# Kernel tuning notes

Hardware: AMD Instinct MI355X
Metric: run time of the kernel (lower is better)

Reference implementation:

```python
import jax, jax.numpy as jnp
import numpy as np

NUM_CLASS = 10000
FEATURE_DIM = 512
PARAM = 0.5


def _xavier_uniform(key, shape):
    fan_out, fan_in = shape
    bound = float(np.sqrt(6.0 / (fan_in + fan_out)))
    return jax.random.uniform(key, shape, jnp.float32, -bound, bound)


def setup_inputs() -> dict:
    key = jax.random.key(0)
    k1, k2, k3, k4, k5 = jax.random.split(key, 5)
    B = 4096
    soft_x = jax.random.normal(k1, (B, FEATURE_DIM), jnp.float32)
    hard_x = jax.random.normal(k2, (B, FEATURE_DIM), jnp.float32)
    targets = jax.random.randint(k3, (B,), 0, NUM_CLASS, jnp.int64)
    centers = _xavier_uniform(k4, (NUM_CLASS, FEATURE_DIM))
    weight = _xavier_uniform(k5, (NUM_CLASS, FEATURE_DIM))
    return {"soft_x": soft_x, "hard_x": hard_x, "targets": targets,
            "centers": centers, "weight": weight}


def _cross_entropy(logits, targets):
    # mean over batch of -log_softmax(logits)[target]
    logp = jax.nn.log_softmax(logits, axis=-1)
    return -jnp.mean(jnp.take_along_axis(logp, targets[:, None], axis=-1))


def reference(soft_x, hard_x, targets, centers, weight):
    # [B, C] logits via GEMM (F.linear -> x @ W^T)
    soft_pred = soft_x @ weight.T
    hard_pred = hard_x @ weight.T
    loss_cls1 = _cross_entropy(soft_pred, targets)
    loss_cls2 = _cross_entropy(hard_pred, targets)
    # Quantization loss: per-class loop == per-sample gather of centers
    c = centers[targets]                                # [B, D]
    quant = 0.5 * (jnp.sum((soft_x - c) ** 2) + jnp.sum((hard_x - c) ** 2))
    loss = loss_cls1 + loss_cls2 + PARAM * quant / soft_x.shape[0]
    return loss
```

## Files before the change

### kernel.cpp

```cpp
#include <hip/hip_runtime.h>
#include <stdint.h>

#define NUM_CLASS 10000
#define FEATDIM   512
#define BATCH     4096
#define MROWS     8192
#define BM        128
#define BN        128
#define NTILES    79
#define NSPLIT    12
#define ROWTILES  64
#define WPAD_ROWS 10112
#define ROWB4     256
#define KBLKS     16

#define PB_CVTX   512
#define PB_CVTW   632
#define PB_ROWS   1024
#define PB_ZERO   8
#define PB_TOTAL  (PB_CVTX + PB_CVTW + PB_ROWS + PB_ZERO)

typedef float f32x4 __attribute__((ext_vector_type(4)));
typedef int   i32x8 __attribute__((ext_vector_type(8)));

__device__ __forceinline__ void gll16(const void* g, void* l) {
  __builtin_amdgcn_global_load_lds(
      (const __attribute__((address_space(1))) void*)g,
      (__attribute__((address_space(3))) void*)l,
      16, 0, 0);
}

__device__ __forceinline__ unsigned q1(float v, float rs) {
  float a = fabsf(v) * rs;
  unsigned s = (__float_as_uint(v) >> 31) << 3;
  unsigned c = a < 0.25f ? 0u : a < 0.75f ? 1u : a < 1.25f ? 2u : a < 1.75f ? 3u
             : a < 2.5f  ? 4u : a < 3.5f  ? 5u : a < 5.0f  ? 6u : 7u;
  return s | c;
}

__device__ __forceinline__ void quant32(const float4* __restrict__ src,
                                        uint4* __restrict__ dst,
                                        unsigned char* __restrict__ sdst) {
  float4 v[8];
#pragma unroll
  for (int i = 0; i < 8; ++i) v[i] = src[i];
  float m = 0.f;
#pragma unroll
  for (int i = 0; i < 8; ++i) {
    m = fmaxf(m, fmaxf(fmaxf(fabsf(v[i].x), fabsf(v[i].y)),
                       fmaxf(fabsf(v[i].z), fabsf(v[i].w))));
  }
  unsigned sb; float rs;
  if (m == 0.f) { sb = 0u; rs = 0.f; }
  else {
    int e = (int)ceilf(log2f(m * 0.16666667f) - 1e-6f);
    e = e < -126 ? -126 : (e > 127 ? 127 : e);
    sb = (unsigned)(e + 127);
    rs = __uint_as_float((unsigned)(127 - e) << 23);
  }
  unsigned wd[4] = {0u, 0u, 0u, 0u};
#pragma unroll
  for (int i = 0; i < 8; ++i) {
    unsigned hw = q1(v[i].x, rs) | (q1(v[i].y, rs) << 4) |
                  (q1(v[i].z, rs) << 8) | (q1(v[i].w, rs) << 12);
    wd[i >> 1] |= hw << ((i & 1) * 16);
  }
  uint4 o = {wd[0], wd[1], wd[2], wd[3]};
  *dst = o;
  *sdst = (unsigned char)sb;
}

__device__ __forceinline__ int spos(int row, int blk) {
  return row * 16 + (blk & 3) * 4 + (blk >> 2);
}

__global__ void prep_kernel(const float* __restrict__ sx, const float* __restrict__ hx,
                            const int* __restrict__ tgt,
                            const float* __restrict__ centers,
                            const float* __restrict__ weight,
                            uint4* __restrict__ X4, uint4* __restrict__ W4,
                            unsigned char* __restrict__ SX, unsigned char* __restrict__ SW,
                            float* __restrict__ tlogit, float* __restrict__ qrow,
                            float4* __restrict__ sumexp4) {
  const int b   = blockIdx.x;
  const int tid = threadIdx.x;

  if (b < PB_CVTX) {
    int idx = b * 256 + tid;
    int row = idx >> 4, blk = idx & 15;
    const float* base = (row < BATCH) ? sx : hx;
    int r = (row < BATCH) ? row : row - BATCH;
    const float4* src = (const float4*)(base + (size_t)r * FEATDIM) + blk * 8;
    quant32(src, &X4[idx], &SX[spos(row, blk)]);
    return;
  }
  if (b < PB_CVTX + PB_CVTW) {
    int idx = (b - PB_CVTX) * 256 + tid;
    int row = idx >> 4, blk = idx & 15;
    if (row < NUM_CLASS) {
      const float4* src = (const float4*)(weight + (size_t)row * FEATDIM) + blk * 8;
      quant32(src, &W4[idx], &SW[spos(row, blk)]);
    } else {
      uint4 z = {0u, 0u, 0u, 0u};
      W4[idx] = z;
      SW[spos(row, blk)] = 0;
    }
    return;
  }
  if (b < PB_CVTX + PB_CVTW + PB_ROWS) {
    int row  = (b - PB_CVTX - PB_CVTW) * 4 + (tid >> 6);
    int lane = tid & 63;
    int t = tgt[row];
    const float4* s4 = (const float4*)(sx + (size_t)row * FEATDIM);
    const float4* h4 = (const float4*)(hx + (size_t)row * FEATDIM);
    const float4* c4 = (const float4*)(centers + (size_t)t * FEATDIM);
    const float4* w4 = (const float4*)(weight + (size_t)t * FEATDIM);
    float qs = 0.f, ds = 0.f, dh = 0.f;
#pragma unroll
    for (int j = 0; j < 2; ++j) {
      int i = lane + j * 64;
      float4 s = s4[i], h = h4[i], c = c4[i], w = w4[i];
      float d0 = s.x - c.x, d1 = s.y - c.y, d2 = s.z - c.z, d3 = s.w - c.w;
      float e0 = h.x - c.x, e1 = h.y - c.y, e2 = h.z - c.z, e3 = h.w - c.w;
      qs += d0*d0 + d1*d1 + d2*d2 + d3*d3 + e0*e0 + e1*e1 + e2*e2 + e3*e3;
      ds += s.x*w.x + s.y*w.y + s.z*w.z + s.w*w.w;
      dh += h.x*w.x + h.y*w.y + h.z*w.z + h.w*w.w;
    }
#pragma unroll
    for (int m = 1; m < 64; m <<= 1) {
      qs += __shfl_xor(qs, m);
      ds += __shfl_xor(ds, m);
      dh += __shfl_xor(dh, m);
    }
    if (lane == 0) {
      tlogit[row]         = ds;
      tlogit[BATCH + row] = dh;
      qrow[row]           = qs;
    }
    return;
  }
  {
    int idx = (b - PB_CVTX - PB_CVTW - PB_ROWS) * 256 + tid;
    float4 z = {0.f, 0.f, 0.f, 0.f};
    sumexp4[idx] = z;
  }
}

__device__ __forceinline__ i32x8 mk8(uint4 q) {
  i32x8 v;
  v[0] = (int)q.x; v[1] = (int)q.y; v[2] = (int)q.z; v[3] = (int)q.w;
  v[4] = 0; v[5] = 0; v[6] = 0; v[7] = 0;
  return v;
}

__launch_bounds__(256, 3)
__global__ void gemm_lse_kernel(const char* __restrict__ X4, const char* __restrict__ W4,
                                const unsigned* __restrict__ SX,
                                const unsigned* __restrict__ SW,
                                float* __restrict__ sumexp) {
  __shared__ char ldsA[2][BM * 64];
  __shared__ char ldsB[2][BN * 64];

  const int tid  = threadIdx.x;
  const int lane = tid & 63;
  const int w    = tid >> 6;
  const int wm   = w >> 1;
  const int wn   = w & 1;
  const int chunk   = blockIdx.x >> 6;
  const int rowtile = blockIdx.x & 63;
  const int nt0 = (chunk * NTILES) / NSPLIT;
  const int nt1 = ((chunk + 1) * NTILES) / NSPLIT;

  const int arow0 = rowtile * BM;
  const int rl = lane & 15;
  const int h  = lane >> 4;
  const int rcol = ((h ^ ((rl >> 1) & 3)) << 4);
  const int scol = (((lane & 3) ^ ((lane >> 3) & 3)) << 4);

  int srowit[4], ssubit[4], sdstit[4];
#pragma unroll
  for (int it = 0; it < 4; ++it) {
    int sub = it >> 1, k = it & 1;
    int segq = w * 2 + k;
    srowit[it] = segq * 16 + (lane >> 2);
    ssubit[it] = sub;
    sdstit[it] = segq * 1024 + lane * 16;
  }
  size_t aoff[4];
#pragma unroll
  for (int it = 0; it < 4; ++it)
    aoff[it] = (size_t)(arow0 + srowit[it]) * ROWB4 + ssubit[it] * 64 + scol;

  unsigned sa4[4];
#pragma unroll
  for (int mi = 0; mi < 4; ++mi)
    sa4[mi] = SX[(arow0 + wm * 64 + mi * 16 + rl) * 4 + h];

  float se[4][4];
#pragma unroll
  for (int mi = 0; mi < 4; ++mi)
#pragma unroll
    for (int r = 0; r < 4; ++r) se[mi][r] = 0.f;

  for (int nt = nt0; nt < nt1; ++nt) {
    const int brow0 = nt * BN;

    unsigned sb4[4];
#pragma unroll
    for (int ni = 0; ni < 4; ++ni)
      sb4[ni] = SW[(brow0 + wn * 64 + ni * 16 + rl) * 4 + h];

    size_t boff[4];
#pragma unroll
    for (int it = 0; it < 4; ++it)
      boff[it] = (size_t)(brow0 + srowit[it]) * ROWB4 + ssubit[it] * 64 + scol;

    f32x4 acc[4][4];
#pragma unroll
    for (int mi = 0; mi < 4; ++mi)
#pragma unroll
      for (int ni = 0; ni < 4; ++ni) {
        f32x4 z = {0.f, 0.f, 0.f, 0.f};
        acc[mi][ni] = z;
      }

#pragma unroll
    for (int h2 = 0; h2 < 2; ++h2) {
      __syncthreads();
#pragma unroll
      for (int it = 0; it < 4; ++it)
        gll16(X4 + aoff[it] + h2 * 128, ldsA[ssubit[it]] + sdstit[it]);
#pragma unroll
      for (int it = 0; it < 4; ++it)
        gll16(W4 + boff[it] + h2 * 128, ldsB[ssubit[it]] + sdstit[it]);
      __syncthreads();

#pragma unroll
      for (int ks2 = 0; ks2 < 2; ++ks2) {
        const int ks = h2 * 2 + ks2;
        uint4 aq[4], bq[4];
#pragma unroll
        for (int mi = 0; mi < 4; ++mi)
          aq[mi] = *(const uint4*)(ldsA[ks2] + (wm * 64 + mi * 16 + rl) * 64 + rcol);
#pragma unroll
        for (int ni = 0; ni < 4; ++ni)
          bq[ni] = *(const uint4*)(ldsB[ks2] + (wn * 64 + ni * 16 + rl) * 64 + rcol);

        int saks[4], sbks[4];
#pragma unroll
        for (int mi = 0; mi < 4; ++mi) saks[mi] = (int)((sa4[mi] >> (ks * 8)) & 0xFFu);
#pragma unroll
        for (int ni = 0; ni < 4; ++ni) sbks[ni] = (int)((sb4[ni] >> (ks * 8)) & 0xFFu);

        i32x8 bv[4];
#pragma unroll
        for (int ni = 0; ni < 4; ++ni) bv[ni] = mk8(bq[ni]);
#pragma unroll
        for (int mi = 0; mi < 4; ++mi) {
          i32x8 av = mk8(aq[mi]);
#pragma unroll
          for (int ni = 0; ni < 4; ++ni)
            acc[mi][ni] = __builtin_amdgcn_mfma_scale_f32_16x16x128_f8f6f4(
                av, bv[ni], acc[mi][ni],
                4, 4,
                0, saks[mi], 0, sbks[ni]);
        }
      }
    }

    const int colb = nt * BN + wn * 64 + rl;
#pragma unroll
    for (int ni = 0; ni < 4; ++ni) {
      bool ok = (colb + ni * 16) < NUM_CLASS;
#pragma unroll
      for (int mi = 0; mi < 4; ++mi)
#pragma unroll
        for (int r = 0; r < 4; ++r)
          if (ok) se[mi][r] += __expf(acc[mi][ni][r]);
    }
  }

#pragma unroll
  for (int m = 1; m < 16; m <<= 1)
#pragma unroll
    for (int mi = 0; mi < 4; ++mi)
#pragma unroll
      for (int r = 0; r < 4; ++r)
        se[mi][r] += __shfl_xor(se[mi][r], m);

  if ((lane & 15) == 0) {
#pragma unroll
    for (int mi = 0; mi < 4; ++mi)
#pragma unroll
      for (int r = 0; r < 4; ++r) {
        int grow = arow0 + wm * 64 + mi * 16 + ((lane >> 4) << 2) + r;
        atomicAdd(&sumexp[grow], se[mi][r]);
      }
  }
}

__global__ void finalize_kernel(const float* __restrict__ sumexp,
                                const float* __restrict__ tlogit,
                                const float* __restrict__ qrow,
                                float* __restrict__ out) {
  int tid = threadIdx.x;
  float acc = 0.f, q = 0.f;
  for (int i = tid; i < MROWS; i += 1024)
    acc += logf(sumexp[i]) - tlogit[i];
  for (int i = tid; i < BATCH; i += 1024)
    q += qrow[i];
#pragma unroll
  for (int m = 1; m < 64; m <<= 1) {
    acc += __shfl_xor(acc, m);
    q   += __shfl_xor(q, m);
  }
  __shared__ float redA[16], redQ[16];
  if ((tid & 63) == 0) { redA[tid >> 6] = acc; redQ[tid >> 6] = q; }
  __syncthreads();
  if (tid == 0) {
    float s = 0.f, qq = 0.f;
#pragma unroll
    for (int i = 0; i < 16; ++i) { s += redA[i]; qq += redQ[i]; }
    out[0] = s * (1.0f / BATCH) + qq * (1.0f / 16384.0f);
  }
}

extern "C" void kernel_launch(void* const* d_in, const int* in_sizes, int n_in,
                              void* d_out, int out_size, void* d_ws, size_t ws_size,
                              hipStream_t stream) {
  const float* sx = (const float*)d_in[0];
  const float* hx = (const float*)d_in[1];
  const int*   tg = (const int*)d_in[2];
  const float* ct = (const float*)d_in[3];
  const float* wt = (const float*)d_in[4];
  float* out = (float*)d_out;

  char* ws = (char*)d_ws;
  char* X4 = ws;
  char* W4 = X4 + (size_t)MROWS * ROWB4;
  unsigned char* SX = (unsigned char*)(W4 + (size_t)WPAD_ROWS * ROWB4);
  unsigned char* SW = SX + (size_t)MROWS * KBLKS;
  char* tail = (char*)(SW + (size_t)WPAD_ROWS * KBLKS);
  float* sumexp = (float*)tail;
  float* tlogit = (float*)(tail + (size_t)MROWS * 4);
  float* qrow   = (float*)(tail + (size_t)MROWS * 8);

  prep_kernel<<<PB_TOTAL, 256, 0, stream>>>(sx, hx, tg, ct, wt,
                                            (uint4*)X4, (uint4*)W4, SX, SW,
                                            tlogit, qrow, (float4*)sumexp);
  gemm_lse_kernel<<<NSPLIT * ROWTILES, 256, 0, stream>>>(X4, W4,
                                                         (const unsigned*)SX,
                                                         (const unsigned*)SW, sumexp);
  finalize_kernel<<<1, 1024, 0, stream>>>(sumexp, tlogit, qrow, out);
}
```

Measured before the change: 61.07 us.

## Overlap exp epilogue of previous tile with next tile's global loads

```diff
diff --git a/kernel.cpp b/kernel.cpp
--- a/kernel.cpp
+++ b/kernel.cpp
@@ -170,6 +170,7 @@
   const int rowtile = blockIdx.x & 63;
   const int nt0 = (chunk * NTILES) / NSPLIT;
   const int nt1 = ((chunk + 1) * NTILES) / NSPLIT;
+  const int G   = (nt1 - nt0) * 2;
 
   const int arow0 = rowtile * BM;
   const int rl = lane & 15;
@@ -202,73 +203,90 @@
 #pragma unroll
     for (int r = 0; r < 4; ++r) se[mi][r] = 0.f;
 
-  for (int nt = nt0; nt < nt1; ++nt) {
-    const int brow0 = nt * BN;
-
-    unsigned sb4[4];
-#pragma unroll
-    for (int ni = 0; ni < 4; ++ni)
-      sb4[ni] = SW[(brow0 + wn * 64 + ni * 16 + rl) * 4 + h];
-
-    size_t boff[4];
-#pragma unroll
-    for (int it = 0; it < 4; ++it)
-      boff[it] = (size_t)(brow0 + srowit[it]) * ROWB4 + ssubit[it] * 64 + scol;
-
-    f32x4 acc[4][4];
-#pragma unroll
-    for (int mi = 0; mi < 4; ++mi)
-#pragma unroll
-      for (int ni = 0; ni < 4; ++ni) {
-        f32x4 z = {0.f, 0.f, 0.f, 0.f};
-        acc[mi][ni] = z;
-      }
-
-#pragma unroll
-    for (int h2 = 0; h2 < 2; ++h2) {
-      __syncthreads();
+  f32x4 acc[4][4];
+  unsigned sb4[4];
+
+  for (int g = 0; g < G; ++g) {
+    const int h2 = g & 1;
+    const int nt = nt0 + (g >> 1);
+
+    __syncthreads();
+
+    {
+      const int brow0 = nt * BN;
 #pragma unroll
       for (int it = 0; it < 4; ++it)
         gll16(X4 + aoff[it] + h2 * 128, ldsA[ssubit[it]] + sdstit[it]);
 #pragma unroll
       for (int it = 0; it < 4; ++it)
-        gll16(W4 + boff[it] + h2 * 128, ldsB[ssubit[it]] + sdstit[it]);
-      __syncthreads();
-
-#pragma unroll
-      for (int ks2 = 0; ks2 < 2; ++ks2) {
-        const int ks = h2 * 2 + ks2;
-        uint4 aq[4], bq[4];
-#pragma unroll
-        for (int mi = 0; mi < 4; ++mi)
-          aq[mi] = *(const uint4*)(ldsA[ks2] + (wm * 64 + mi * 16 + rl) * 64 + rcol);
-#pragma unroll
-        for (int ni = 0; ni < 4; ++ni)
-          bq[ni] = *(const uint4*)(ldsB[ks2] + (wn * 64 + ni * 16 + rl) * 64 + rcol);
-
-        int saks[4], sbks[4];
-#pragma unroll
-        for (int mi = 0; mi < 4; ++mi) saks[mi] = (int)((sa4[mi] >> (ks * 8)) & 0xFFu);
-#pragma unroll
-        for (int ni = 0; ni < 4; ++ni) sbks[ni] = (int)((sb4[ni] >> (ks * 8)) & 0xFFu);
-
-        i32x8 bv[4];
-#pragma unroll
-        for (int ni = 0; ni < 4; ++ni) bv[ni] = mk8(bq[ni]);
-#pragma unroll
-        for (int mi = 0; mi < 4; ++mi) {
-          i32x8 av = mk8(aq[mi]);
-#pragma unroll
-          for (int ni = 0; ni < 4; ++ni)
-            acc[mi][ni] = __builtin_amdgcn_mfma_scale_f32_16x16x128_f8f6f4(
-                av, bv[ni], acc[mi][ni],
-                4, 4,
-                0, saks[mi], 0, sbks[ni]);
+        gll16(W4 + (size_t)(brow0 + srowit[it]) * ROWB4 + ssubit[it] * 64 + scol
+                 + h2 * 128,
+              ldsB[ssubit[it]] + sdstit[it]);
+    }
+
+    if (h2 == 0) {
+      if (g > 0) {
+        const int colb = (nt - 1) * BN + wn * 64 + rl;
+#pragma unroll
+        for (int ni = 0; ni < 4; ++ni) {
+          bool ok = (colb + ni * 16) < NUM_CLASS;
+#pragma unroll
+          for (int mi = 0; mi < 4; ++mi)
+#pragma unroll
+            for (int r = 0; r < 4; ++r)
+              if (ok) se[mi][r] += __expf(acc[mi][ni][r]);
         }
       }
-    }
-
-    const int colb = nt * BN + wn * 64 + rl;
+#pragma unroll
+      for (int ni = 0; ni < 4; ++ni)
+        sb4[ni] = SW[(nt * BN + wn * 64 + ni * 16 + rl) * 4 + h];
+#pragma unroll
+      for (int mi = 0; mi < 4; ++mi)
+#pragma unroll
+        for (int ni = 0; ni < 4; ++ni) {
+          f32x4 z = {0.f, 0.f, 0.f, 0.f};
+          acc[mi][ni] = z;
+        }
+    }
+
+    __builtin_amdgcn_sched_barrier(0);
+    __syncthreads();
+
+#pragma unroll
+    for (int ks2 = 0; ks2 < 2; ++ks2) {
+      const int ks = h2 * 2 + ks2;
+      uint4 aq[4], bq[4];
+#pragma unroll
+      for (int mi = 0; mi < 4; ++mi)
+        aq[mi] = *(const uint4*)(ldsA[ks2] + (wm * 64 + mi * 16 + rl) * 64 + rcol);
+#pragma unroll
+      for (int ni = 0; ni < 4; ++ni)
+        bq[ni] = *(const uint4*)(ldsB[ks2] + (wn * 64 + ni * 16 + rl) * 64 + rcol);
+
+      int saks[4], sbks[4];
+#pragma unroll
+      for (int mi = 0; mi < 4; ++mi) saks[mi] = (int)((sa4[mi] >> (ks * 8)) & 0xFFu);
+#pragma unroll
+      for (int ni = 0; ni < 4; ++ni) sbks[ni] = (int)((sb4[ni] >> (ks * 8)) & 0xFFu);
+
+      i32x8 bv[4];
+#pragma unroll
+      for (int ni = 0; ni < 4; ++ni) bv[ni] = mk8(bq[ni]);
+#pragma unroll
+      for (int mi = 0; mi < 4; ++mi) {
+        i32x8 av = mk8(aq[mi]);
+#pragma unroll
+        for (int ni = 0; ni < 4; ++ni)
+          acc[mi][ni] = __builtin_amdgcn_mfma_scale_f32_16x16x128_f8f6f4(
+              av, bv[ni], acc[mi][ni],
+              4, 4,
+              0, saks[mi], 0, sbks[ni]);
+      }
+    }
+  }
+
+  {
+    const int colb = (nt1 - 1) * BN + wn * 64 + rl;
 #pragma unroll
     for (int ni = 0; ni < 4; ++ni) {
       bool ok = (colb + ni * 16) < NUM_CLASS;
```

Measured after the change: 62.05 us, median of 2. No clear change (+1.6%).
